# Performance work log

Hardware: AMD Instinct MI355X
Metric: run time of the kernel (lower is better)

The kernel has to match this reference:

```python
import math
import jax, jax.numpy as jnp
import numpy as np

# model config (matches init_kwargs)
V, D, DC, DM, DE, DG, H, L, TMAX = 32000, 1024, 512, 1024, 4096, 1024, 16, 6, 2048
CHD = max(1, DC // H)   # q/k head dim = 32
MHD = max(1, DM // H)   # v head dim   = 64
B, T = 2, 1024
EPS = 1e-5


def setup_inputs() -> dict:
    key = jax.random.key(0)
    ks = iter(jax.random.split(key, 40))
    s = 0.02
    rn = lambda shape: jax.random.normal(next(ks), shape, dtype=jnp.float32) * s
    inp = {
        'ids': jax.random.randint(next(ks), (B, T), 0, V),
        'te': rn((V, D)),            # tied token embedding / lm head weight
        'pe': rn((TMAX, D)),
        # per-layer stacked params, leading dim L
        'ln1_g': jnp.ones((L, D)), 'ln1_b': jnp.zeros((L, D)),
        'qp_w': rn((L, D, H * CHD)), 'qp_b': jnp.zeros((L, H * CHD)),
        'kp_w': rn((L, D, H * CHD)), 'kp_b': jnp.zeros((L, H * CHD)),
        'vp_w': rn((L, D, H * MHD)), 'vp_b': jnp.zeros((L, H * MHD)),
        'out_w': rn((L, H * MHD, D)), 'out_b': jnp.zeros((L, D)),
        'ln2_g': jnp.ones((L, D)), 'ln2_b': jnp.zeros((L, D)),
        'exp_w': rn((L, D, DE)), 'exp_b': jnp.zeros((L, DE)),
        'gate_w': rn((L, D, DG)), 'gate_b': jnp.zeros((L, DG)),
        'gup_w': rn((L, DG, DE)), 'gup_b': jnp.zeros((L, DE)),
        'comp_w': rn((L, DE, D)), 'comp_b': jnp.zeros((L, D)),
        'lnf_g': jnp.ones((D,)), 'lnf_b': jnp.zeros((D,)),
    }
    return inp


def _ln(x, g, b):
    m = jnp.mean(x, axis=-1, keepdims=True)
    v = jnp.mean(jnp.square(x - m), axis=-1, keepdims=True)
    return (x - m) * jax.lax.rsqrt(v + EPS) * g + b


def _forward(ids, te, pe, ln1_g, ln1_b, qp_w, qp_b, kp_w, kp_b, vp_w, vp_b,
             out_w, out_b, ln2_g, ln2_b, exp_w, exp_b, gate_w, gate_b,
             gup_w, gup_b, comp_w, comp_b, lnf_g, lnf_b):
    b, t = ids.shape
    x = te[ids] + pe[jnp.arange(t)][None, :, :]          # [B,T,D]
    causal = jnp.tril(jnp.ones((t, t), dtype=bool))       # [T,T]
    scale = 1.0 / math.sqrt(CHD)

    def block(x, p):
        (l1g, l1b, qw, qb, kw, kb, vw, vb, ow, ob,
         l2g, l2b, ew, eb, gw, gb, guw, gub, cw, cb) = p
        # --- attention sublayer ---
        h = _ln(x, l1g, l1b)
        q = (h @ qw + qb).reshape(b, t, H, CHD)
        k = (h @ kw + kb).reshape(b, t, H, CHD)
        v = (h @ vw + vb).reshape(b, t, H, MHD)
        sc = jnp.einsum('bqhd,bkhd->bhqk', q, k) * scale
        sc = jnp.where(causal[None, None], sc, -jnp.inf)
        a = jax.nn.softmax(sc, axis=-1)
        y = jnp.einsum('bhqk,bkhd->bqhd', a, v).reshape(b, t, H * MHD)
        x = x + y @ ow + ob
        # --- gated FFN sublayer ---
        h2 = _ln(x, l2g, l2b)
        e = h2 @ ew + eb
        g = jax.nn.sigmoid(jax.nn.silu(h2 @ gw + gb) @ guw + gub)
        x = x + jax.nn.silu(e * g) @ cw + cb
        return x, None

    params = (ln1_g, ln1_b, qp_w, qp_b, kp_w, kp_b, vp_w, vp_b, out_w, out_b,
              ln2_g, ln2_b, exp_w, exp_b, gate_w, gate_b, gup_w, gup_b,
              comp_w, comp_b)
    x, _ = jax.lax.scan(block, x, params)
    logits = _ln(x, lnf_g, lnf_b) @ te.T                  # tied head, [B,T,V]
    return logits


def reference(ids, te, pe, ln1_g, ln1_b, qp_w, qp_b, kp_w, kp_b, vp_w, vp_b,
              out_w, out_b, ln2_g, ln2_b, exp_w, exp_b, gate_w, gate_b,
              gup_w, gup_b, comp_w, comp_b, lnf_g, lnf_b):
    return _forward(ids, te, pe, ln1_g, ln1_b, qp_w, qp_b, kp_w, kp_b,
                    vp_w, vp_b, out_w, out_b, ln2_g, ln2_b, exp_w, exp_b,
                    gate_w, gate_b, gup_w, gup_b, comp_w, comp_b,
                    lnf_g, lnf_b)
```

## Files before the change

kernel.cpp:

```cpp
#include <hip/hip_runtime.h>
#include <math.h>

typedef unsigned short u16;
typedef unsigned int   u32;
typedef __attribute__((ext_vector_type(4))) float f32x4;
typedef __attribute__((ext_vector_type(8))) short s16x8;

#define D_   1024
#define DE_  4096
#define H_   16
#define CHD_ 32
#define MHD_ 64
#define L_   6
#define B_   2
#define T_   1024
#define M_   (B_*T_)
#define V_   32000
#define EPS_ 1e-5f

__device__ __forceinline__ float bf2f(u16 u){ return __uint_as_float(((u32)u) << 16); }
__device__ __forceinline__ u16 f2bf(float f){
    u32 x = __float_as_uint(f);
    return (u16)((x + 0x7fffu + ((x >> 16) & 1u)) >> 16);
}
__device__ __forceinline__ float ldf(const void* p, size_t i, int f16){
    return f16 ? bf2f(((const u16*)p)[i]) : ((const float*)p)[i];
}
__device__ __forceinline__ float sigf(float x){ return 1.f / (1.f + __expf(-x)); }

typedef __attribute__((address_space(3))) u32 as3_u32;
typedef const __attribute__((address_space(1))) u32 as1_u32;
__device__ __forceinline__ void gld16(const void* g, void* l){
    __builtin_amdgcn_global_load_lds((as1_u32*)g, (as3_u32*)l, 16, 0, 0);
}
__device__ __forceinline__ int swz(int row){ return (row >> 1) & 3; }

__global__ void detect_dtype(const u16* __restrict__ te_u16, int* __restrict__ flag){
    __shared__ int any_big;
    if (threadIdx.x == 0) any_big = 0;
    __syncthreads();
    int big = 0;
    #pragma unroll
    for (int i=0;i<4;i++){
        u16 u = te_u16[threadIdx.x + 256*i];
        int e = (u >> 7) & 0xFF;
        if (e >= 0x88) big = 1;
    }
    if (big) any_big = 1;
    __syncthreads();
    if (threadIdx.x == 0) *flag = any_big ? 0 : 1;
}

__global__ __launch_bounds__(256) void conv_te(const void* __restrict__ te,
        u16* __restrict__ dst, const int* __restrict__ flagp){
    int f16 = *flagp;
    size_t i = ((size_t)blockIdx.x*256 + threadIdx.x)*8;
    if (f16){
        *(s16x8*)(dst+i) = *(const s16x8*)((const u16*)te + i);
    } else {
        const float* s = (const float*)te + i;
        float4 f0 = *(const float4*)s, f1 = *(const float4*)(s+4);
        s16x8 pk;
        pk[0]=(short)f2bf(f0.x); pk[1]=(short)f2bf(f0.y);
        pk[2]=(short)f2bf(f0.z); pk[3]=(short)f2bf(f0.w);
        pk[4]=(short)f2bf(f1.x); pk[5]=(short)f2bf(f1.y);
        pk[6]=(short)f2bf(f1.z); pk[7]=(short)f2bf(f1.w);
        *(s16x8*)(dst+i) = pk;
    }
}

__global__ __launch_bounds__(256) void embed_kernel(const int* __restrict__ ids,
        const void* __restrict__ te, const void* __restrict__ pe,
        float* __restrict__ x, const int* __restrict__ flagp){
    int f16 = *flagp;
    int idx = blockIdx.x*256 + threadIdx.x;
    int m = idx >> 10, d = idx & 1023;
    int t = m & (T_-1);
    x[idx] = ldf(te, (size_t)ids[m]*D_ + d, f16) + ldf(pe, (size_t)t*D_ + d, f16);
}

__device__ __forceinline__ float blk_sum(float v, float* smem){
    #pragma unroll
    for (int o=32;o>0;o>>=1) v += __shfl_xor(v, o);
    __syncthreads();
    if ((threadIdx.x & 63) == 0) smem[threadIdx.x>>6] = v;
    __syncthreads();
    return smem[0]+smem[1]+smem[2]+smem[3];
}

__global__ __launch_bounds__(256) void ln_kernel(const float* __restrict__ x,
        const void* __restrict__ g, const void* __restrict__ b, size_t goff,
        u16* __restrict__ out, const int* __restrict__ flagp){
    __shared__ float smem[4];
    int f16 = *flagp;
    int row = blockIdx.x, tid = threadIdx.x;
    const float* xr = x + (size_t)row*D_;
    float v[4]; float s = 0.f;
    #pragma unroll
    for (int i=0;i<4;i++){ v[i] = xr[tid+256*i]; s += v[i]; }
    float mean = blk_sum(s, smem) * (1.f/D_);
    float vs = 0.f;
    #pragma unroll
    for (int i=0;i<4;i++){ float d = v[i]-mean; vs += d*d; }
    float inv = rsqrtf(blk_sum(vs, smem)*(1.f/D_) + EPS_);
    u16* orow = out + (size_t)row*D_;
    #pragma unroll
    for (int i=0;i<4;i++){
        int c = tid+256*i;
        orow[c] = f2bf((v[i]-mean)*inv*ldf(g, goff+c, f16) + ldf(b, goff+c, f16));
    }
}

__global__ __launch_bounds__(256) void wt_tr(
        const void* s0, size_t o0, u16* d0,
        const void* s1, size_t o1, u16* d1,
        const void* s2, size_t o2, u16* d2,
        int K, int N, const int* __restrict__ flagp){
    const void* s; size_t o; u16* d;
    if (blockIdx.z == 0){ s=s0; o=o0; d=d0; }
    else if (blockIdx.z == 1){ s=s1; o=o1; d=d1; }
    else { s=s2; o=o2; d=d2; }
    int f16 = *flagp;
    __shared__ float tile[32][33];
    int k0 = blockIdx.y*32, n0 = blockIdx.x*32;
    int c = threadIdx.x & 31, r8 = threadIdx.x >> 5;
    #pragma unroll
    for (int i=0;i<4;i++){
        int r = r8 + i*8;
        tile[r][c] = ldf(s, o + (size_t)(k0+r)*N + n0 + c, f16);
    }
    __syncthreads();
    #pragma unroll
    for (int i=0;i<4;i++){
        int r = r8 + i*8;
        d[(size_t)(n0+r)*K + k0 + c] = f2bf(tile[c][r]);
    }
}

__global__ __launch_bounds__(256) void v_transpose(const u16* __restrict__ qkv,
                                                   u16* __restrict__ vt){
    __shared__ u16 tile[32][34];
    int bh = blockIdx.z, b = bh >> 4, h = bh & 15;
    int t0 = blockIdx.x*32, d0 = blockIdx.y*32;
    int c = threadIdx.x & 31, r8 = threadIdx.x >> 5;
    #pragma unroll
    for (int i=0;i<4;i++){
        int r = r8 + i*8;
        tile[r][c] = qkv[(size_t)(b*T_ + t0 + r)*2048 + 1024 + h*64 + d0 + c];
    }
    __syncthreads();
    #pragma unroll
    for (int i=0;i<4;i++){
        int r = r8 + i*8;
        vt[(size_t)(bh*64 + d0 + r)*T_ + t0 + c] = tile[c][r];
    }
}

__global__ __launch_bounds__(256) void bias_cat(
        const void* qb_, const void* kb_, const void* vb_,
        const void* eb_, const void* gb_,
        size_t oq, size_t ok, size_t ov, size_t oe, size_t og,
        float* __restrict__ b1, float* __restrict__ b2,
        const int* __restrict__ flagp){
    int f16 = *flagp;
    int i = blockIdx.x*256 + threadIdx.x;
    if (i < 2048){
        float v = (i < 512)  ? ldf(qb_, oq + i, f16)
                : (i < 1024) ? ldf(kb_, ok + i - 512, f16)
                :              ldf(vb_, ov + i - 1024, f16);
        b1[i] = v;
    } else {
        int j = i - 2048;
        float v = (j < DE_) ? ldf(eb_, oe + j, f16)
                            : ldf(gb_, og + j - DE_, f16);
        b2[j] = v;
    }
}

template<int MODE, bool RESID, bool BIASF32, int TN, int SK>
__global__ __launch_bounds__(256) void gemm_mfma(
        const u16* __restrict__ A, int lda,
        const void* __restrict__ B, int ldb,
        const void* __restrict__ bias, size_t boff,
        void* __restrict__ C, int ldc,
        int N, int K, const int* __restrict__ flagp){
    constexpr int MT = (TN == 128) ? 4 : 2;
    constexpr int NT = 4;
    __shared__ __align__(16) char smem[8192 + TN*64];
    char* ldsA = smem;
    char* ldsB = smem + 8192;
    const int t = threadIdx.x;
    const int w = t >> 6, lane = t & 63;
    const int fr = lane & 15, g = lane >> 4;
    const int wm = (TN == 128) ? (w >> 1) * 64 : w * 32;
    const int wn = (TN == 128) ? (w & 1) * 64 : 0;

    const int gx = gridDim.x, gy = gridDim.y;
    const int nwg = gx * gy;
    const int lin = blockIdx.y * gx + blockIdx.x;
    const int neu = (lin & 7) * (nwg >> 3) + (lin >> 3);
    const int m0 = (neu % gy) * 128;
    const int n0 = (neu / gy) * TN;

    const int f16 = *flagp;
    const bool convB = (MODE == 3) && !f16;

    const int srow = t >> 2, sslot = t & 3;
    const int aslot = sslot ^ swz(srow);
    const u16* srcA   = A + (size_t)(m0 + srow) * lda + 8 * aslot;
    const u16* srcB16 = (const u16*)B + (size_t)(n0 + srow) * ldb + 8 * aslot;
    const int crow = t >> 1;
    const int cs0 = (t & 1) * 2;
    const float* srcBf = (const float*)B + (size_t)(n0 + crow) * ldb;

    char* dstA = ldsA + w * 1024;
    char* dstB = ldsB + w * 1024;

    f32x4 acc[MT][NT];
    const f32x4 zero = {0.f, 0.f, 0.f, 0.f};
    #pragma unroll
    for (int i=0;i<MT;i++)
        #pragma unroll
        for (int j=0;j<NT;j++) acc[i][j] = zero;

    const int slotb = (g ^ swz(fr)) * 16;

    const int kps  = K / SK;
    const int kbeg = (SK > 1) ? blockIdx.z * kps : 0;
    const int kend = kbeg + kps;

    for (int k0 = kbeg; k0 < kend; k0 += 32){
        gld16(srcA + k0,                      dstA);
        gld16(srcA + k0 + (size_t)64 * lda,   dstA + 4096);
        if (!convB){
            gld16(srcB16 + k0, dstB);
            if (TN == 128)
                gld16(srcB16 + k0 + (size_t)64 * ldb, dstB + 4096);
        } else {
            #pragma unroll
            for (int si=0; si<2; si++){
                int s = cs0 + si;
                const float* sp = srcBf + k0 + 8 * (s ^ swz(crow));
                float4 f0 = *(const float4*)sp;
                float4 f1 = *(const float4*)(sp + 4);
                s16x8 pk;
                pk[0]=(short)f2bf(f0.x); pk[1]=(short)f2bf(f0.y);
                pk[2]=(short)f2bf(f0.z); pk[3]=(short)f2bf(f0.w);
                pk[4]=(short)f2bf(f1.x); pk[5]=(short)f2bf(f1.y);
                pk[6]=(short)f2bf(f1.z); pk[7]=(short)f2bf(f1.w);
                *(s16x8*)(ldsB + crow*64 + s*16) = pk;
            }
        }
        __syncthreads();
        s16x8 a[MT], b[NT];
        #pragma unroll
        for (int mt=0;mt<MT;mt++)
            a[mt] = *(const s16x8*)(ldsA + (wm + mt*16 + fr)*64 + slotb);
        #pragma unroll
        for (int nt=0;nt<NT;nt++)
            b[nt] = *(const s16x8*)(ldsB + (wn + nt*16 + fr)*64 + slotb);
        #pragma unroll
        for (int mt=0;mt<MT;mt++)
            #pragma unroll
            for (int nt=0;nt<NT;nt++)
                acc[mt][nt] = __builtin_amdgcn_mfma_f32_16x16x32_bf16(
                                  a[mt], b[nt], acc[mt][nt], 0, 0, 0);
        __syncthreads();
    }

    const bool addb = (SK == 1) || (blockIdx.z == 0);
    #pragma unroll
    for (int nt=0;nt<NT;nt++){
        const int nc = n0 + wn + nt*16 + fr;
        float bv = 0.f;
        if (MODE != 3 && MODE != 5 && addb)
            bv = BIASF32 ? ((const float*)bias)[boff + nc]
                         : ldf(bias, boff + nc, f16);
        #pragma unroll
        for (int mt=0;mt<MT;mt++){
            #pragma unroll
            for (int r=0;r<4;r++){
                const int mr = m0 + wm + mt*16 + g*4 + r;
                const size_t idx = (size_t)mr * ldc + nc;
                float val = acc[mt][nt][r] + bv;
                if (MODE == 4){
                    if (nc >= DE_) val = val * sigf(val);
                    ((u16*)C)[idx] = f2bf(val);
                } else if (MODE == 2){
                    float e = bf2f(((const u16*)C)[idx]);
                    float z = e * sigf(val);
                    ((u16*)C)[idx] = f2bf(z * sigf(z));
                } else if (MODE == 3 || MODE == 5){
                    if (f16) ((u16*)C)[idx] = f2bf(val);
                    else     ((float*)C)[idx] = val;
                } else if (RESID){
                    if (SK > 1) unsafeAtomicAdd(&((float*)C)[idx], val);
                    else        ((float*)C)[idx] += val;
                } else {
                    ((u16*)C)[idx] = f2bf(val);
                }
            }
        }
    }
}

__global__ __launch_bounds__(256) void attn_mfma(const u16* __restrict__ qkv,
                                                 const u16* __restrict__ vt,
                                                 u16* __restrict__ y){
    __shared__ __align__(16) char smem[21504];
    char* ldsK = smem;
    char* ldsV = smem + 4096;
    char* ldsP = smem + 12288;

    const int qt = gridDim.x - 1 - blockIdx.x;
    const int h = blockIdx.y, b = blockIdx.z;
    const int t = threadIdx.x, w = t >> 6, lane = t & 63;
    const int fr = lane & 15, g = lane >> 4;
    const int q0 = qt * 64;
    const int qw = q0 + w * 16;
    const int bh = b * H_ + h;

    const int srow = t >> 2, sslot = t & 3;
    const u16* srcK = qkv + (size_t)(b*T_ + srow)*2048 + 512 + h*32
                      + 8 * (sslot ^ swz(srow));
    const int vrow = t >> 3, vslot = t & 7;
    const u16* srcV0 = vt + (size_t)(bh*64 + vrow)*T_      + 8 * (vslot ^ (vrow & 7));
    const u16* srcV1 = vt + (size_t)(bh*64 + 32 + vrow)*T_ + 8 * (vslot ^ (vrow & 7));

    s16x8 qf = *(const s16x8*)(qkv + (size_t)(b*T_ + qw + fr)*2048 + h*32 + g*8);

    char* pbase = ldsP + w * 2304;

    f32x4 o[4]; float m[4], l[4];
    #pragma unroll
    for (int f=0; f<4; f++) o[f] = (f32x4){0.f,0.f,0.f,0.f};
    #pragma unroll
    for (int r=0; r<4; r++){ m[r] = -3.0e38f; l[r] = 0.f; }

    const float scale = 0.17677669529663687f;
    const f32x4 zero = {0.f,0.f,0.f,0.f};

    for (int j0 = 0; j0 < q0 + 64; j0 += 64){
        __syncthreads();
        gld16(srcK + (size_t)j0*2048, ldsK + w*1024);
        gld16(srcV0 + j0,             ldsV + w*1024);
        gld16(srcV1 + j0,             ldsV + 4096 + w*1024);
        __syncthreads();
        if (j0 <= qw + 15){
            f32x4 s[4];
            #pragma unroll
            for (int f=0; f<4; f++){
                int row = f*16 + fr;
                s16x8 kf = *(const s16x8*)(ldsK + row*64 + (g ^ swz(row))*16);
                s[f] = __builtin_amdgcn_mfma_f32_16x16x32_bf16(qf, kf, zero, 0,0,0);
            }
            bool needmask = (j0 + 63 > qw);
            #pragma unroll
            for (int f=0; f<4; f++){
                int j = j0 + f*16 + fr;
                #pragma unroll
                for (int r=0; r<4; r++){
                    float sv = s[f][r] * scale;
                    if (needmask && j > qw + g*4 + r) sv = -3.0e38f;
                    s[f][r] = sv;
                }
            }
            float mx[4];
            #pragma unroll
            for (int r=0; r<4; r++)
                mx[r] = fmaxf(fmaxf(s[0][r], s[1][r]), fmaxf(s[2][r], s[3][r]));
            #pragma unroll
            for (int o2=8; o2>0; o2>>=1)
                #pragma unroll
                for (int r=0; r<4; r++) mx[r] = fmaxf(mx[r], __shfl_xor(mx[r], o2));
            float al[4];
            #pragma unroll
            for (int r=0; r<4; r++){
                float mn = fmaxf(m[r], mx[r]);
                al[r] = __expf(m[r] - mn);
                m[r] = mn;
            }
            float ps[4] = {0.f,0.f,0.f,0.f};
            #pragma unroll
            for (int f=0; f<4; f++)
                #pragma unroll
                for (int r=0; r<4; r++){
                    float p = __expf(s[f][r] - m[r]);
                    ps[r] += p;
                    *(u16*)(pbase + (g*4+r)*144 + (fr + 16*f)*2) = f2bf(p);
                }
            #pragma unroll
            for (int o2=8; o2>0; o2>>=1)
                #pragma unroll
                for (int r=0; r<4; r++) ps[r] += __shfl_xor(ps[r], o2);
            #pragma unroll
            for (int r=0; r<4; r++) l[r] = l[r]*al[r] + ps[r];
            #pragma unroll
            for (int f=0; f<4; f++)
                #pragma unroll
                for (int r=0; r<4; r++) o[f][r] *= al[r];
            #pragma unroll
            for (int kk=0; kk<2; kk++){
                s16x8 pa = *(const s16x8*)(pbase + fr*144 + kk*64 + g*16);
                #pragma unroll
                for (int f=0; f<4; f++){
                    int row = f*16 + fr;
                    s16x8 vb = *(const s16x8*)(ldsV + row*128 + (((kk*4+g) ^ (row&7))*16));
                    o[f] = __builtin_amdgcn_mfma_f32_16x16x32_bf16(pa, vb, o[f], 0,0,0);
                }
            }
        }
    }
    #pragma unroll
    for (int r=0; r<4; r++){
        float inv = 1.f / l[r];
        u16* yr = y + (size_t)(b*T_ + qw + g*4 + r)*1024 + h*64;
        #pragma unroll
        for (int f=0; f<4; f++)
            yr[fr + 16*f] = f2bf(o[f][r] * inv);
    }
}

extern "C" void kernel_launch(void* const* d_in, const int* in_sizes, int n_in,
                              void* d_out, int out_size, void* d_ws, size_t ws_size,
                              hipStream_t stream){
    const int*  ids   = (const int*) d_in[0];
    const void* te    = d_in[1];
    const void* pe    = d_in[2];
    const void* ln1_g = d_in[3];
    const void* ln1_b = d_in[4];
    const void* qp_w  = d_in[5];
    const void* qp_b  = d_in[6];
    const void* kp_w  = d_in[7];
    const void* kp_b  = d_in[8];
    const void* vp_w  = d_in[9];
    const void* vp_b  = d_in[10];
    const void* out_w = d_in[11];
    const void* out_b = d_in[12];
    const void* ln2_g = d_in[13];
    const void* ln2_b = d_in[14];
    const void* exp_w = d_in[15];
    const void* exp_b = d_in[16];
    const void* gate_w= d_in[17];
    const void* gate_b= d_in[18];
    const void* gup_w = d_in[19];
    const void* gup_b = d_in[20];
    const void* comp_w= d_in[21];
    const void* comp_b= d_in[22];
    const void* lnf_g = d_in[23];
    const void* lnf_b = d_in[24];

    char* ws = (char*)d_ws;
    int*   flag  = (int*)ws;
    float* bcat1 = (float*)(ws + 4096);
    float* bcat2 = (float*)(ws + 4096 + 8192);
    float* x     = (float*)(ws + (1u<<20));
    u16*   hb    = (u16*)  (ws + (9u<<20));
    u16*   qkvb  = (u16*)  (ws + (13u<<20));
    u16*   yb    = (u16*)  (ws + (21u<<20));
    u16*   vtb   = (u16*)  (ws + (25u<<20));
    u16*   eg1   = (u16*)  (ws + (13u<<20));
    u16*   wb    = (u16*)  (ws + (33u<<20));
    u16*   te16  = (u16*)  (ws + ((size_t)44<<20));

    const size_t need = ((size_t)44<<20) + (size_t)V_*D_*2 + (1u<<20);
    const bool pre = (ws_size >= need);

    detect_dtype<<<1, 256, 0, stream>>>((const u16*)te, flag);
    if (pre)
        conv_te<<<(V_*D_)/2048, 256, 0, stream>>>(te, te16, flag);
    embed_kernel<<<(M_*D_)/256, 256, 0, stream>>>(ids, te, pe, x, flag);

    for (int l=0; l<L_; l++){
        size_t lD = (size_t)l*D_;
        wt_tr<<<dim3(16,32,2), 256, 0, stream>>>(
            qp_w, (size_t)l*D_*512, wb,
            kp_w, (size_t)l*D_*512, wb + (size_t)512*1024,
            nullptr, 0, nullptr, 1024, 512, flag);
        wt_tr<<<dim3(32,32,2), 256, 0, stream>>>(
            vp_w,  (size_t)l*D_*1024,  wb + (size_t)1024*1024,
            out_w, (size_t)l*1024*1024, wb + (size_t)2048*1024,
            nullptr, 0, nullptr, 1024, 1024, flag);
        bias_cat<<<28, 256, 0, stream>>>(qp_b, kp_b, vp_b, exp_b, gate_b,
            (size_t)l*512, (size_t)l*512, (size_t)l*1024,
            (size_t)l*DE_, (size_t)l*1024, bcat1, bcat2, flag);

        ln_kernel<<<M_, 256, 0, stream>>>(x, ln1_g, ln1_b, lD, hb, flag);
        gemm_mfma<0,false,true,64,1><<<dim3(32,16), 256, 0, stream>>>(
            hb, 1024, wb, 1024, bcat1, 0, qkvb, 2048, 2048, 1024, flag);
        v_transpose<<<dim3(32,2,32), 256, 0, stream>>>(qkvb, vtb);
        attn_mfma<<<dim3(T_/64, H_, B_), 256, 0, stream>>>(qkvb, vtb, yb);
        gemm_mfma<0,true,false,64,2><<<dim3(16,16,2), 256, 0, stream>>>(
            yb, 1024, wb + (size_t)2048*1024, 1024,
            out_b, (size_t)l*1024, x, 1024, 1024, 1024, flag);

        wt_tr<<<dim3(128,32,1), 256, 0, stream>>>(
            exp_w, (size_t)l*D_*DE_, wb,
            nullptr,0,nullptr, nullptr,0,nullptr, 1024, 4096, flag);
        wt_tr<<<dim3(32,32,1), 256, 0, stream>>>(
            gate_w, (size_t)l*D_*1024, wb + (size_t)4096*1024,
            nullptr,0,nullptr, nullptr,0,nullptr, 1024, 1024, flag);
        ln_kernel<<<M_, 256, 0, stream>>>(x, ln2_g, ln2_b, lD, hb, flag);
        gemm_mfma<4,false,true,128,1><<<dim3(40,16), 256, 0, stream>>>(
            hb, 1024, wb, 1024, bcat2, 0, eg1, 5120, 5120, 1024, flag);
        wt_tr<<<dim3(128,32,1), 256, 0, stream>>>(
            gup_w, (size_t)l*1024*DE_, wb,
            nullptr,0,nullptr, nullptr,0,nullptr, 1024, 4096, flag);
        gemm_mfma<2,false,false,128,1><<<dim3(32,16), 256, 0, stream>>>(
            eg1 + 4096, 5120, wb, 1024,
            gup_b, (size_t)l*DE_, eg1, 5120, 4096, 1024, flag);
        wt_tr<<<dim3(32,128,1), 256, 0, stream>>>(
            comp_w, (size_t)l*DE_*1024, wb,
            nullptr,0,nullptr, nullptr,0,nullptr, 4096, 1024, flag);
        gemm_mfma<0,true,false,64,2><<<dim3(16,16,2), 256, 0, stream>>>(
            eg1, 5120, wb, 4096, comp_b, (size_t)l*1024, x, 1024, 1024, 4096, flag);
    }

    ln_kernel<<<M_, 256, 0, stream>>>(x, lnf_g, lnf_b, 0, hb, flag);
    if (pre)
        gemm_mfma<5,false,false,128,1><<<dim3(V_/128, M_/128), 256, 0, stream>>>(
            hb, 1024, te16, 1024, nullptr, 0, d_out, V_, V_, 1024, flag);
    else
        gemm_mfma<3,false,false,128,1><<<dim3(V_/128, M_/128), 256, 0, stream>>>(
            hb, 1024, te, 1024, nullptr, 0, d_out, V_, V_, 1024, flag);
}
```

Measured before the change: 2.398 ms.

## Double GEMM K-tile to 64 and widen weight-transpose tiles with vector I/O

The GEMM kernel now stages 64 K-elements per iteration instead of 32, using a 128-byte swizzled LDS row layout and two MFMA sub-steps per barrier pair. This halves the number of loop iterations and __syncthreads, at the cost of doubling LDS use per block, which may reduce occupancy. The weight-transpose kernel moves to 64x64 tiles with float4 reads for fp32 input and 16-byte vector bf16 stores, cutting per-element global accesses. Launch grids are adjusted to match.

```diff
diff --git a/kernel.cpp b/kernel.cpp
--- a/kernel.cpp
+++ b/kernel.cpp
@@ -121,20 +121,36 @@
     else if (blockIdx.z == 1){ s=s1; o=o1; d=d1; }
     else { s=s2; o=o2; d=d2; }
     int f16 = *flagp;
-    __shared__ float tile[32][33];
-    int k0 = blockIdx.y*32, n0 = blockIdx.x*32;
-    int c = threadIdx.x & 31, r8 = threadIdx.x >> 5;
-    #pragma unroll
-    for (int i=0;i<4;i++){
-        int r = r8 + i*8;
-        tile[r][c] = ldf(s, o + (size_t)(k0+r)*N + n0 + c, f16);
+    __shared__ float tile[64][65];
+    int k0 = blockIdx.y*64, n0 = blockIdx.x*64;
+    int t = threadIdx.x;
+    if (!f16){
+        int c4 = (t & 15)*4, r = t >> 4;
+        const float* S = (const float*)s + o + (size_t)(k0 + r)*N + n0 + c4;
+        #pragma unroll
+        for (int i=0;i<4;i++){
+            float4 v = *(const float4*)(S + (size_t)(16*i)*N);
+            tile[r+16*i][c4+0] = v.x; tile[r+16*i][c4+1] = v.y;
+            tile[r+16*i][c4+2] = v.z; tile[r+16*i][c4+3] = v.w;
+        }
+    } else {
+        int c = t & 63, r4 = t >> 6;
+        #pragma unroll
+        for (int i=0;i<16;i++){
+            int r = r4 + i*4;
+            tile[r][c] = bf2f(((const u16*)s)[o + (size_t)(k0+r)*N + n0 + c]);
+        }
     }
     __syncthreads();
-    #pragma unroll
-    for (int i=0;i<4;i++){
-        int r = r8 + i*8;
-        d[(size_t)(n0+r)*K + k0 + c] = f2bf(tile[c][r]);
-    }
+    int n = t >> 2, kq = (t & 3)*16;
+    s16x8 lo, hi;
+    #pragma unroll
+    for (int i=0;i<8;i++) lo[i] = (short)f2bf(tile[kq+i][n]);
+    #pragma unroll
+    for (int i=0;i<8;i++) hi[i] = (short)f2bf(tile[kq+8+i][n]);
+    u16* D = d + (size_t)(n0+n)*K + k0 + kq;
+    *(s16x8*)D = lo;
+    *(s16x8*)(D+8) = hi;
 }
 
 __global__ __launch_bounds__(256) void v_transpose(const u16* __restrict__ qkv,
@@ -186,9 +202,10 @@
         int N, int K, const int* __restrict__ flagp){
     constexpr int MT = (TN == 128) ? 4 : 2;
     constexpr int NT = 4;
-    __shared__ __align__(16) char smem[8192 + TN*64];
+    constexpr int BCALLS = TN / 32;
+    __shared__ __align__(16) char smem[16384 + TN*128];
     char* ldsA = smem;
-    char* ldsB = smem + 8192;
+    char* ldsB = smem + 16384;
     const int t = threadIdx.x;
     const int w = t >> 6, lane = t & 63;
     const int fr = lane & 15, g = lane >> 4;
@@ -205,12 +222,10 @@
     const int f16 = *flagp;
     const bool convB = (MODE == 3) && !f16;
 
-    const int srow = t >> 2, sslot = t & 3;
-    const int aslot = sslot ^ swz(srow);
-    const u16* srcA   = A + (size_t)(m0 + srow) * lda + 8 * aslot;
-    const u16* srcB16 = (const u16*)B + (size_t)(n0 + srow) * ldb + 8 * aslot;
-    const int crow = t >> 1;
-    const int cs0 = (t & 1) * 2;
+    const int srow = t >> 3, sslot = t & 7;
+    const u16* srcA   = A + (size_t)(m0 + srow) * lda + 8 * (sslot ^ (srow & 7));
+    const u16* srcB16 = (const u16*)B + (size_t)(n0 + srow) * ldb + 8 * (sslot ^ (srow & 7));
+    const int crow = t >> 1, chalf = t & 1;
     const float* srcBf = (const float*)B + (size_t)(n0 + crow) * ldb;
 
     char* dstA = ldsA + w * 1024;
@@ -222,25 +237,24 @@
     for (int i=0;i<MT;i++)
         #pragma unroll
         for (int j=0;j<NT;j++) acc[i][j] = zero;
-
-    const int slotb = (g ^ swz(fr)) * 16;
 
     const int kps  = K / SK;
     const int kbeg = (SK > 1) ? blockIdx.z * kps : 0;
     const int kend = kbeg + kps;
 
-    for (int k0 = kbeg; k0 < kend; k0 += 32){
-        gld16(srcA + k0,                      dstA);
-        gld16(srcA + k0 + (size_t)64 * lda,   dstA + 4096);
+    for (int k0 = kbeg; k0 < kend; k0 += 64){
+        #pragma unroll
+        for (int i=0;i<4;i++)
+            gld16(srcA + (size_t)(32*i)*lda + k0, dstA + i*4096);
         if (!convB){
-            gld16(srcB16 + k0, dstB);
-            if (TN == 128)
-                gld16(srcB16 + k0 + (size_t)64 * ldb, dstB + 4096);
+            #pragma unroll
+            for (int i=0;i<BCALLS;i++)
+                gld16(srcB16 + (size_t)(32*i)*ldb + k0, dstB + i*4096);
         } else {
             #pragma unroll
-            for (int si=0; si<2; si++){
-                int s = cs0 + si;
-                const float* sp = srcBf + k0 + 8 * (s ^ swz(crow));
+            for (int s4=0;s4<4;s4++){
+                int sl = chalf*4 + s4;
+                const float* sp = srcBf + k0 + 8*(sl ^ (crow & 7));
                 float4 f0 = *(const float4*)sp;
                 float4 f1 = *(const float4*)(sp + 4);
                 s16x8 pk;
@@ -248,23 +262,27 @@
                 pk[2]=(short)f2bf(f0.z); pk[3]=(short)f2bf(f0.w);
                 pk[4]=(short)f2bf(f1.x); pk[5]=(short)f2bf(f1.y);
                 pk[6]=(short)f2bf(f1.z); pk[7]=(short)f2bf(f1.w);
-                *(s16x8*)(ldsB + crow*64 + s*16) = pk;
+                *(s16x8*)(ldsB + crow*128 + sl*16) = pk;
             }
         }
         __syncthreads();
-        s16x8 a[MT], b[NT];
-        #pragma unroll
-        for (int mt=0;mt<MT;mt++)
-            a[mt] = *(const s16x8*)(ldsA + (wm + mt*16 + fr)*64 + slotb);
-        #pragma unroll
-        for (int nt=0;nt<NT;nt++)
-            b[nt] = *(const s16x8*)(ldsB + (wn + nt*16 + fr)*64 + slotb);
-        #pragma unroll
-        for (int mt=0;mt<MT;mt++)
+        #pragma unroll
+        for (int kk=0;kk<2;kk++){
+            const int so = ((kk*4 + g) ^ (fr & 7)) * 16;
+            s16x8 a[MT], b[NT];
+            #pragma unroll
+            for (int mt=0;mt<MT;mt++)
+                a[mt] = *(const s16x8*)(ldsA + (wm + mt*16 + fr)*128 + so);
             #pragma unroll
             for (int nt=0;nt<NT;nt++)
-                acc[mt][nt] = __builtin_amdgcn_mfma_f32_16x16x32_bf16(
-                                  a[mt], b[nt], acc[mt][nt], 0, 0, 0);
+                b[nt] = *(const s16x8*)(ldsB + (wn + nt*16 + fr)*128 + so);
+            #pragma unroll
+            for (int mt=0;mt<MT;mt++)
+                #pragma unroll
+                for (int nt=0;nt<NT;nt++)
+                    acc[mt][nt] = __builtin_amdgcn_mfma_f32_16x16x32_bf16(
+                                      a[mt], b[nt], acc[mt][nt], 0, 0, 0);
+        }
         __syncthreads();
     }
 
@@ -473,11 +491,11 @@
 
     for (int l=0; l<L_; l++){
         size_t lD = (size_t)l*D_;
-        wt_tr<<<dim3(16,32,2), 256, 0, stream>>>(
+        wt_tr<<<dim3(8,16,2), 256, 0, stream>>>(
             qp_w, (size_t)l*D_*512, wb,
             kp_w, (size_t)l*D_*512, wb + (size_t)512*1024,
             nullptr, 0, nullptr, 1024, 512, flag);
-        wt_tr<<<dim3(32,32,2), 256, 0, stream>>>(
+        wt_tr<<<dim3(16,16,2), 256, 0, stream>>>(
             vp_w,  (size_t)l*D_*1024,  wb + (size_t)1024*1024,
             out_w, (size_t)l*1024*1024, wb + (size_t)2048*1024,
             nullptr, 0, nullptr, 1024, 1024, flag);
@@ -494,22 +512,22 @@
             yb, 1024, wb + (size_t)2048*1024, 1024,
             out_b, (size_t)l*1024, x, 1024, 1024, 1024, flag);
 
-        wt_tr<<<dim3(128,32,1), 256, 0, stream>>>(
+        wt_tr<<<dim3(64,16,1), 256, 0, stream>>>(
             exp_w, (size_t)l*D_*DE_, wb,
             nullptr,0,nullptr, nullptr,0,nullptr, 1024, 4096, flag);
-        wt_tr<<<dim3(32,32,1), 256, 0, stream>>>(
+        wt_tr<<<dim3(16,16,1), 256, 0, stream>>>(
             gate_w, (size_t)l*D_*1024, wb + (size_t)4096*1024,
             nullptr,0,nullptr, nullptr,0,nullptr, 1024, 1024, flag);
         ln_kernel<<<M_, 256, 0, stream>>>(x, ln2_g, ln2_b, lD, hb, flag);
         gemm_mfma<4,false,true,128,1><<<dim3(40,16), 256, 0, stream>>>(
             hb, 1024, wb, 1024, bcat2, 0, eg1, 5120, 5120, 1024, flag);
-        wt_tr<<<dim3(128,32,1), 256, 0, stream>>>(
+        wt_tr<<<dim3(64,16,1), 256, 0, stream>>>(
             gup_w, (size_t)l*1024*DE_, wb,
             nullptr,0,nullptr, nullptr,0,nullptr, 1024, 4096, flag);
         gemm_mfma<2,false,false,128,1><<<dim3(32,16), 256, 0, stream>>>(
             eg1 + 4096, 5120, wb, 1024,
             gup_b, (size_t)l*DE_, eg1, 5120, 4096, 1024, flag);
-        wt_tr<<<dim3(32,128,1), 256, 0, stream>>>(
+        wt_tr<<<dim3(16,64,1), 256, 0, stream>>>(
             comp_w, (size_t)l*DE_*1024, wb,
             nullptr,0,nullptr, nullptr,0,nullptr, 4096, 1024, flag);
         gemm_mfma<0,true,false,64,2><<<dim3(16,16,2), 256, 0, stream>>>(
```

Result: faster. 2.170 ms (-9.5%).
